# Kernel optimization log

Hardware: AMD Instinct MI355X
Metric: run time of the kernel (lower is better)

Reference implementation:

```python
import jax, jax.numpy as jnp
import numpy as np

B, N, IN_DIM, HID = 16, 1024, 2, 64
GDEP = 2
ALPHA = 3.0                      # DGCRM/DGCN tanh alpha
GC_ALPHA, GC_BETA, GC_GAMMA = 0.05, 0.95, 0.95  # list_weight
HYPER, MID, NODE_DIM = 32, 16, 40
CIN = HID + IN_DIM               # 66
CAT = (GDEP + 1) * CIN           # 198


def setup_inputs() -> dict:
    key = jax.random.key(0)
    ks = jax.random.split(key, 14)
    x = jax.random.normal(ks[0], (B, N, IN_DIM), jnp.float32)
    hidden_state = 0.1 * jax.random.normal(ks[1], (B, N, HID), jnp.float32)
    nodevec1 = jax.random.normal(ks[2], (N, NODE_DIM), jnp.float32)
    nodevec2 = jax.random.normal(ks[3], (N, NODE_DIM), jnp.float32)
    A0 = jax.random.uniform(ks[4], (N, N), jnp.float32)
    A0 = A0 / A0.sum(-1, keepdims=True)
    A1 = jax.random.uniform(ks[5], (N, N), jnp.float32)
    A1 = A1 / A1.sum(-1, keepdims=True)
    s = 0.05  # small init scale
    hyper_W1 = s * jax.random.normal(ks[6], (4, CAT, HYPER), jnp.float32)
    hyper_b1 = jnp.zeros((4, HYPER), jnp.float32)
    hyper_W2 = s * jax.random.normal(ks[7], (4, HYPER, MID), jnp.float32)
    hyper_b2 = jnp.zeros((4, MID), jnp.float32)
    hyper_W3 = s * jax.random.normal(ks[8], (4, MID, NODE_DIM), jnp.float32)
    hyper_b3 = jnp.zeros((4, NODE_DIM), jnp.float32)
    rnn_W = s * jax.random.normal(ks[9], (6, CAT, HID), jnp.float32)
    rnn_b = jnp.zeros((6, HID), jnp.float32)
    return dict(x=x, hidden_state=hidden_state, nodevec1=nodevec1, nodevec2=nodevec2,
                A0=A0, A1=A1, hyper_W1=hyper_W1, hyper_b1=hyper_b1,
                hyper_W2=hyper_W2, hyper_b2=hyper_b2, hyper_W3=hyper_W3,
                hyper_b3=hyper_b3, rnn_W=rnn_W, rnn_b=rnn_b)


def reference(x, hidden_state, nodevec1, nodevec2, A0, A1,
              hyper_W1, hyper_b1, hyper_W2, hyper_b2, hyper_W3, hyper_b3,
              rnn_W, rnn_b):
    def gconv_hyper(inp, adj, i):
        # K-hop diffusion: h = alpha*x + gamma * (h^T adj) over node dim
        h = inp
        outs = [h]
        for _ in range(GDEP):
            h = GC_ALPHA * inp + GC_GAMMA * jnp.einsum('bnc,nm->bmc', h, adj)
            outs.append(h)
        ho = jnp.concatenate(outs, axis=-1)           # [B,N,(gdep+1)*CIN]
        ho = jax.nn.sigmoid(ho @ hyper_W1[i] + hyper_b1[i])
        ho = jax.nn.sigmoid(ho @ hyper_W2[i] + hyper_b2[i])
        return ho @ hyper_W3[i] + hyper_b3[i]         # [B,N,NODE_DIM]

    def gconv_rnn(inp, i):
        # FAITHFUL to source bug: stray leading '+' makes the beta/gamma
        # einsum terms standalone no-op statements, so each hop is h=alpha*x.
        outs = [inp] + [GC_ALPHA * inp] * GDEP
        return jnp.concatenate(outs, axis=-1) @ rnn_W[i] + rnn_b[i]

    # --- DGCN: dynamic adjacency generation ---
    hyper_input = jnp.concatenate((x, hidden_state), axis=-1)  # [B,N,CIN]
    filter1 = gconv_hyper(hyper_input, A0, 0) + gconv_hyper(hyper_input, A1, 1)
    filter2 = gconv_hyper(hyper_input, A0, 2) + gconv_hyper(hyper_input, A1, 3)
    nv1 = jnp.tanh(ALPHA * nodevec1[None] * filter1)  # [B,N,NODE_DIM]
    nv2 = jnp.tanh(ALPHA * nodevec2[None] * filter2)
    a = jnp.einsum('bnd,bmd->bnm', nv1, nv2) - jnp.einsum('bnd,bmd->bnm', nv2, nv1)
    adp_raw = jax.nn.relu(jnp.tanh(ALPHA * a))        # [B,N,N]
    eye = jnp.eye(N, dtype=adp_raw.dtype)
    def norm(adj):
        adj = adj + eye
        return adj / adj.sum(-1, keepdims=True)
    adp = norm(adp_raw)                               # computed as in source
    adpT = norm(jnp.swapaxes(adp_raw, 1, 2))          # (unused downstream due to
    del adp, adpT                                     #  the GConv_RNN source bug)

    # --- GRU-style gating ---
    combined = jnp.concatenate((x, hidden_state), axis=-1)
    z = jax.nn.sigmoid(gconv_rnn(combined, 0) + gconv_rnn(combined, 1))
    r = jax.nn.sigmoid(gconv_rnn(combined, 2) + gconv_rnn(combined, 3))
    candidate = jnp.concatenate((x, r * hidden_state), axis=-1)
    hc = jnp.tanh(gconv_rnn(candidate, 4) + gconv_rnn(candidate, 5))
    h = z * hidden_state + (1.0 - z) * hc             # [B,N,HID]
    return h
```

## Files before the change

### kernel.cpp

```cpp
#include <hip/hip_runtime.h>
#include <math.h>

#define NTOK   16384
#define CIN_   66
#define HID_   64
#define NCH    192
#define TPB    32

__device__ __forceinline__ float fast_sigmoid(float a) {
    return 1.0f / (1.0f + __expf(-a));
}
__device__ __forceinline__ float fast_tanh(float a) {
    return 1.0f - 2.0f / (__expf(2.0f * a) + 1.0f);
}

__global__ void fold_weights(const float* __restrict__ rnn_W,
                             const float* __restrict__ rnn_b,
                             float* __restrict__ Wf,
                             float* __restrict__ bf)
{
    int idx = blockIdx.x * blockDim.x + threadIdx.x;
    if (idx >= CIN_ * NCH) return;
    int k = idx / NCH;
    int c = idx - k * NCH;
    int g = c >> 6;
    int j = c & 63;
    int i0 = 2 * g, i1 = 2 * g + 1;
    const float s = 0.05f;
    float v = 0.0f;
    v += rnn_W[(i0 * 198 + k) * 64 + j]
       + s * (rnn_W[(i0 * 198 + 66 + k) * 64 + j] + rnn_W[(i0 * 198 + 132 + k) * 64 + j]);
    v += rnn_W[(i1 * 198 + k) * 64 + j]
       + s * (rnn_W[(i1 * 198 + 66 + k) * 64 + j] + rnn_W[(i1 * 198 + 132 + k) * 64 + j]);
    Wf[k * NCH + c] = v;
    if (k == 0) bf[c] = rnn_b[i0 * 64 + j] + rnn_b[i1 * 64 + j];
}

__global__ __launch_bounds__(256)
void dgcrm_gru(const float* __restrict__ x,
               const float* __restrict__ h,
               const float* __restrict__ Wf,
               const float* __restrict__ bf,
               float* __restrict__ out)
{
    __shared__ float C[CIN_][TPB + 1];
    __shared__ float D[CIN_][TPB + 1];
    __shared__ float Z[HID_][TPB + 1];

    const int tid = threadIdx.x;
    const int t0  = blockIdx.x * TPB;

    {
        const float4* h4 = (const float4*)(h + (size_t)t0 * HID_);
        #pragma unroll
        for (int r = 0; r < 2; ++r) {
            int i = tid + r * 256;
            float4 v = h4[i];
            int f = i * 4;
            int t = f >> 6;
            int c = f & 63;
            C[2 + c + 0][t] = v.x;
            C[2 + c + 1][t] = v.y;
            C[2 + c + 2][t] = v.z;
            C[2 + c + 3][t] = v.w;
        }
    }
    if (tid < 2 * TPB) {
        int t = tid >> 1, k = tid & 1;
        float v = x[(size_t)(t0 + t) * 2 + k];
        C[k][t] = v;
        D[k][t] = v;
    }
    __syncthreads();

    const int grp  = tid >> 4;
    const int tokA = tid & 15;
    const int tokB = tokA + 16;

    {
        const int ch0 = grp * 8;
        float accA[8], accB[8];
        {
            float4 b0 = *(const float4*)(bf + ch0);
            float4 b1 = *(const float4*)(bf + ch0 + 4);
            accA[0] = b0.x; accA[1] = b0.y; accA[2] = b0.z; accA[3] = b0.w;
            accA[4] = b1.x; accA[5] = b1.y; accA[6] = b1.z; accA[7] = b1.w;
            #pragma unroll
            for (int j = 0; j < 8; ++j) accB[j] = accA[j];
        }
        for (int k = 0; k < CIN_; ++k) {
            float ckA = C[k][tokA];
            float ckB = C[k][tokB];
            const float4* w4 = (const float4*)(Wf + k * NCH + ch0);
            float4 w0 = w4[0];
            float4 w1 = w4[1];
            accA[0] = fmaf(ckA, w0.x, accA[0]);  accB[0] = fmaf(ckB, w0.x, accB[0]);
            accA[1] = fmaf(ckA, w0.y, accA[1]);  accB[1] = fmaf(ckB, w0.y, accB[1]);
            accA[2] = fmaf(ckA, w0.z, accA[2]);  accB[2] = fmaf(ckB, w0.z, accB[2]);
            accA[3] = fmaf(ckA, w0.w, accA[3]);  accB[3] = fmaf(ckB, w0.w, accB[3]);
            accA[4] = fmaf(ckA, w1.x, accA[4]);  accB[4] = fmaf(ckB, w1.x, accB[4]);
            accA[5] = fmaf(ckA, w1.y, accA[5]);  accB[5] = fmaf(ckB, w1.y, accB[5]);
            accA[6] = fmaf(ckA, w1.z, accA[6]);  accB[6] = fmaf(ckB, w1.z, accB[6]);
            accA[7] = fmaf(ckA, w1.w, accA[7]);  accB[7] = fmaf(ckB, w1.w, accB[7]);
        }
        if (grp < 8) {
            #pragma unroll
            for (int j = 0; j < 8; ++j) {
                Z[ch0 + j][tokA] = fast_sigmoid(accA[j]);
                Z[ch0 + j][tokB] = fast_sigmoid(accB[j]);
            }
        } else {
            const int rb = ch0 - 64;
            #pragma unroll
            for (int j = 0; j < 8; ++j) {
                D[2 + rb + j][tokA] = fast_sigmoid(accA[j]) * C[2 + rb + j][tokA];
                D[2 + rb + j][tokB] = fast_sigmoid(accB[j]) * C[2 + rb + j][tokB];
            }
        }
    }
    __syncthreads();

    {
        const int c0 = 128 + grp * 4;
        float accA[4], accB[4];
        {
            float4 b0 = *(const float4*)(bf + c0);
            accA[0] = b0.x; accA[1] = b0.y; accA[2] = b0.z; accA[3] = b0.w;
            #pragma unroll
            for (int j = 0; j < 4; ++j) accB[j] = accA[j];
        }
        for (int k = 0; k < CIN_; ++k) {
            float dkA = D[k][tokA];
            float dkB = D[k][tokB];
            float4 w = *(const float4*)(Wf + k * NCH + c0);
            accA[0] = fmaf(dkA, w.x, accA[0]);  accB[0] = fmaf(dkB, w.x, accB[0]);
            accA[1] = fmaf(dkA, w.y, accA[1]);  accB[1] = fmaf(dkB, w.y, accB[1]);
            accA[2] = fmaf(dkA, w.z, accA[2]);  accB[2] = fmaf(dkB, w.z, accB[2]);
            accA[3] = fmaf(dkA, w.w, accA[3]);  accB[3] = fmaf(dkB, w.w, accB[3]);
        }
        const int hb = grp * 4;
        #pragma unroll
        for (int j = 0; j < 4; ++j) {
            float hcA = fast_tanh(accA[j]);
            float hcB = fast_tanh(accB[j]);
            float zvA = Z[hb + j][tokA];
            float zvB = Z[hb + j][tokB];
            float hvA = C[2 + hb + j][tokA];
            float hvB = C[2 + hb + j][tokB];
            Z[hb + j][tokA] = zvA * hvA + (1.0f - zvA) * hcA;
            Z[hb + j][tokB] = zvB * hvB + (1.0f - zvB) * hcB;
        }
    }
    __syncthreads();

    {
        float4* o4 = (float4*)(out + (size_t)t0 * HID_);
        #pragma unroll
        for (int r = 0; r < 2; ++r) {
            int i = tid + r * 256;
            int f = i * 4;
            int t = f >> 6;
            int c = f & 63;
            float4 v;
            v.x = Z[c + 0][t];
            v.y = Z[c + 1][t];
            v.z = Z[c + 2][t];
            v.w = Z[c + 3][t];
            o4[i] = v;
        }
    }
}

extern "C" void kernel_launch(void* const* d_in, const int* in_sizes, int n_in,
                              void* d_out, int out_size, void* d_ws, size_t ws_size,
                              hipStream_t stream)
{
    const float* x     = (const float*)d_in[0];
    const float* hprev = (const float*)d_in[1];
    const float* rnn_W = (const float*)d_in[12];
    const float* rnn_b = (const float*)d_in[13];

    float* Wf = (float*)d_ws;
    float* bf = Wf + CIN_ * NCH;

    fold_weights<<<(CIN_ * NCH + 255) / 256, 256, 0, stream>>>(rnn_W, rnn_b, Wf, bf);
    dgcrm_gru<<<NTOK / TPB, 256, 0, stream>>>(x, hprev, Wf, bf, (float*)d_out);
}
```

Measured before the change: 102.3 us.

## Switch shared tiles to token-major with float4 access and regroup folded weights per thread group

Shared-memory staging tiles change from channel-major to token-major with a padded row of 68, so hidden-state loads, gate reads and output stores use float4 accesses instead of scalar transposed ones. Input channels are reordered so the 64 hidden channels come first and the two x channels last. The folded weight matrix is split into per-group contiguous blocks to make each thread group's weight reads sequential. This targets LDS instruction count and scattered weight loads, at the cost of more complex indexing and possible LDS bank conflicts from float4 reads across rows.

```diff
diff --git a/kernel.cpp b/kernel.cpp
--- a/kernel.cpp
+++ b/kernel.cpp
@@ -6,6 +6,10 @@
 #define HID_   64
 #define NCH    192
 #define TPB    32
+#define KPAD   68
+
+#define WT1_ELEMS (16 * 66 * 8)
+#define WT2_ELEMS (16 * 66 * 4)
 
 __device__ __forceinline__ float fast_sigmoid(float a) {
     return 1.0f / (1.0f + __expf(-a));
@@ -16,36 +20,50 @@
 
 __global__ void fold_weights(const float* __restrict__ rnn_W,
                              const float* __restrict__ rnn_b,
-                             float* __restrict__ Wf,
+                             float* __restrict__ Wt1,
+                             float* __restrict__ Wt2,
                              float* __restrict__ bf)
 {
     int idx = blockIdx.x * blockDim.x + threadIdx.x;
     if (idx >= CIN_ * NCH) return;
-    int k = idx / NCH;
-    int c = idx - k * NCH;
+    int knew = idx / NCH;
+    int c    = idx - knew * NCH;
+    int korig = (knew < 64) ? (knew + 2) : (knew - 64);
     int g = c >> 6;
     int j = c & 63;
     int i0 = 2 * g, i1 = 2 * g + 1;
     const float s = 0.05f;
     float v = 0.0f;
-    v += rnn_W[(i0 * 198 + k) * 64 + j]
-       + s * (rnn_W[(i0 * 198 + 66 + k) * 64 + j] + rnn_W[(i0 * 198 + 132 + k) * 64 + j]);
-    v += rnn_W[(i1 * 198 + k) * 64 + j]
-       + s * (rnn_W[(i1 * 198 + 66 + k) * 64 + j] + rnn_W[(i1 * 198 + 132 + k) * 64 + j]);
-    Wf[k * NCH + c] = v;
-    if (k == 0) bf[c] = rnn_b[i0 * 64 + j] + rnn_b[i1 * 64 + j];
+    v += rnn_W[(i0 * 198 + korig) * 64 + j]
+       + s * (rnn_W[(i0 * 198 + 66 + korig) * 64 + j] + rnn_W[(i0 * 198 + 132 + korig) * 64 + j]);
+    v += rnn_W[(i1 * 198 + korig) * 64 + j]
+       + s * (rnn_W[(i1 * 198 + 66 + korig) * 64 + j] + rnn_W[(i1 * 198 + 132 + korig) * 64 + j]);
+
+    if (g < 2) {
+        int ch  = c;
+        int grp = ch >> 3;
+        int jj  = ch & 7;
+        Wt1[(grp * CIN_ + knew) * 8 + jj] = v;
+    } else {
+        int ch  = c - 128;
+        int grp = ch >> 2;
+        int jj  = ch & 3;
+        Wt2[(grp * CIN_ + knew) * 4 + jj] = v;
+    }
+    if (knew == 0) bf[c] = rnn_b[i0 * 64 + j] + rnn_b[i1 * 64 + j];
 }
 
 __global__ __launch_bounds__(256)
 void dgcrm_gru(const float* __restrict__ x,
                const float* __restrict__ h,
-               const float* __restrict__ Wf,
+               const float* __restrict__ Wt1,
+               const float* __restrict__ Wt2,
                const float* __restrict__ bf,
                float* __restrict__ out)
 {
-    __shared__ float C[CIN_][TPB + 1];
-    __shared__ float D[CIN_][TPB + 1];
-    __shared__ float Z[HID_][TPB + 1];
+    __shared__ float Cs[TPB][KPAD];
+    __shared__ float Ds[TPB][KPAD];
+    __shared__ float Zs[TPB][KPAD];
 
     const int tid = threadIdx.x;
     const int t0  = blockIdx.x * TPB;
@@ -56,20 +74,16 @@
         for (int r = 0; r < 2; ++r) {
             int i = tid + r * 256;
             float4 v = h4[i];
-            int f = i * 4;
-            int t = f >> 6;
-            int c = f & 63;
-            C[2 + c + 0][t] = v.x;
-            C[2 + c + 1][t] = v.y;
-            C[2 + c + 2][t] = v.z;
-            C[2 + c + 3][t] = v.w;
+            int t = i >> 4;
+            int c = (i * 4) & 63;
+            *(float4*)&Cs[t][c] = v;
         }
     }
     if (tid < 2 * TPB) {
         int t = tid >> 1, k = tid & 1;
         float v = x[(size_t)(t0 + t) * 2 + k];
-        C[k][t] = v;
-        D[k][t] = v;
+        Cs[t][64 + k] = v;
+        Ds[t][64 + k] = v;
     }
     __syncthreads();
 
@@ -79,6 +93,7 @@
 
     {
         const int ch0 = grp * 8;
+        const float* wp = Wt1 + grp * (CIN_ * 8);
         float accA[8], accB[8];
         {
             float4 b0 = *(const float4*)(bf + ch0);
@@ -88,40 +103,81 @@
             #pragma unroll
             for (int j = 0; j < 8; ++j) accB[j] = accA[j];
         }
-        for (int k = 0; k < CIN_; ++k) {
-            float ckA = C[k][tokA];
-            float ckB = C[k][tokB];
-            const float4* w4 = (const float4*)(Wf + k * NCH + ch0);
-            float4 w0 = w4[0];
-            float4 w1 = w4[1];
-            accA[0] = fmaf(ckA, w0.x, accA[0]);  accB[0] = fmaf(ckB, w0.x, accB[0]);
-            accA[1] = fmaf(ckA, w0.y, accA[1]);  accB[1] = fmaf(ckB, w0.y, accB[1]);
-            accA[2] = fmaf(ckA, w0.z, accA[2]);  accB[2] = fmaf(ckB, w0.z, accB[2]);
-            accA[3] = fmaf(ckA, w0.w, accA[3]);  accB[3] = fmaf(ckB, w0.w, accB[3]);
-            accA[4] = fmaf(ckA, w1.x, accA[4]);  accB[4] = fmaf(ckB, w1.x, accB[4]);
-            accA[5] = fmaf(ckA, w1.y, accA[5]);  accB[5] = fmaf(ckB, w1.y, accB[5]);
-            accA[6] = fmaf(ckA, w1.z, accA[6]);  accB[6] = fmaf(ckB, w1.z, accB[6]);
-            accA[7] = fmaf(ckA, w1.w, accA[7]);  accB[7] = fmaf(ckB, w1.w, accB[7]);
+        #pragma unroll
+        for (int kb = 0; kb < 16; ++kb) {
+            float4 a4 = *(const float4*)&Cs[tokA][4 * kb];
+            float4 b4 = *(const float4*)&Cs[tokB][4 * kb];
+            float ca[4] = {a4.x, a4.y, a4.z, a4.w};
+            float cb[4] = {b4.x, b4.y, b4.z, b4.w};
+            #pragma unroll
+            for (int j = 0; j < 4; ++j) {
+                float4 w0 = *(const float4*)(wp + (4 * kb + j) * 8);
+                float4 w1 = *(const float4*)(wp + (4 * kb + j) * 8 + 4);
+                accA[0] = fmaf(ca[j], w0.x, accA[0]);  accB[0] = fmaf(cb[j], w0.x, accB[0]);
+                accA[1] = fmaf(ca[j], w0.y, accA[1]);  accB[1] = fmaf(cb[j], w0.y, accB[1]);
+                accA[2] = fmaf(ca[j], w0.z, accA[2]);  accB[2] = fmaf(cb[j], w0.z, accB[2]);
+                accA[3] = fmaf(ca[j], w0.w, accA[3]);  accB[3] = fmaf(cb[j], w0.w, accB[3]);
+                accA[4] = fmaf(ca[j], w1.x, accA[4]);  accB[4] = fmaf(cb[j], w1.x, accB[4]);
+                accA[5] = fmaf(ca[j], w1.y, accA[5]);  accB[5] = fmaf(cb[j], w1.y, accB[5]);
+                accA[6] = fmaf(ca[j], w1.z, accA[6]);  accB[6] = fmaf(cb[j], w1.z, accB[6]);
+                accA[7] = fmaf(ca[j], w1.w, accA[7]);  accB[7] = fmaf(cb[j], w1.w, accB[7]);
+            }
+        }
+        {
+            float a64 = Cs[tokA][64], a65 = Cs[tokA][65];
+            float b64 = Cs[tokB][64], b65 = Cs[tokB][65];
+            float4 u0 = *(const float4*)(wp + 64 * 8);
+            float4 u1 = *(const float4*)(wp + 64 * 8 + 4);
+            float4 v0 = *(const float4*)(wp + 65 * 8);
+            float4 v1 = *(const float4*)(wp + 65 * 8 + 4);
+            float wu[8] = {u0.x,u0.y,u0.z,u0.w,u1.x,u1.y,u1.z,u1.w};
+            float wv[8] = {v0.x,v0.y,v0.z,v0.w,v1.x,v1.y,v1.z,v1.w};
+            #pragma unroll
+            for (int j = 0; j < 8; ++j) {
+                accA[j] = fmaf(a64, wu[j], fmaf(a65, wv[j], accA[j]));
+                accB[j] = fmaf(b64, wu[j], fmaf(b65, wv[j], accB[j]));
+            }
         }
         if (grp < 8) {
-            #pragma unroll
-            for (int j = 0; j < 8; ++j) {
-                Z[ch0 + j][tokA] = fast_sigmoid(accA[j]);
-                Z[ch0 + j][tokB] = fast_sigmoid(accB[j]);
-            }
+            float4 za0, za1, zb0, zb1;
+            za0.x = fast_sigmoid(accA[0]); za0.y = fast_sigmoid(accA[1]);
+            za0.z = fast_sigmoid(accA[2]); za0.w = fast_sigmoid(accA[3]);
+            za1.x = fast_sigmoid(accA[4]); za1.y = fast_sigmoid(accA[5]);
+            za1.z = fast_sigmoid(accA[6]); za1.w = fast_sigmoid(accA[7]);
+            zb0.x = fast_sigmoid(accB[0]); zb0.y = fast_sigmoid(accB[1]);
+            zb0.z = fast_sigmoid(accB[2]); zb0.w = fast_sigmoid(accB[3]);
+            zb1.x = fast_sigmoid(accB[4]); zb1.y = fast_sigmoid(accB[5]);
+            zb1.z = fast_sigmoid(accB[6]); zb1.w = fast_sigmoid(accB[7]);
+            *(float4*)&Zs[tokA][ch0]     = za0;
+            *(float4*)&Zs[tokA][ch0 + 4] = za1;
+            *(float4*)&Zs[tokB][ch0]     = zb0;
+            *(float4*)&Zs[tokB][ch0 + 4] = zb1;
         } else {
             const int rb = ch0 - 64;
-            #pragma unroll
-            for (int j = 0; j < 8; ++j) {
-                D[2 + rb + j][tokA] = fast_sigmoid(accA[j]) * C[2 + rb + j][tokA];
-                D[2 + rb + j][tokB] = fast_sigmoid(accB[j]) * C[2 + rb + j][tokB];
-            }
+            float4 ha0 = *(const float4*)&Cs[tokA][rb];
+            float4 ha1 = *(const float4*)&Cs[tokA][rb + 4];
+            float4 hb0 = *(const float4*)&Cs[tokB][rb];
+            float4 hb1 = *(const float4*)&Cs[tokB][rb + 4];
+            float4 da0, da1, db0, db1;
+            da0.x = fast_sigmoid(accA[0]) * ha0.x;  da0.y = fast_sigmoid(accA[1]) * ha0.y;
+            da0.z = fast_sigmoid(accA[2]) * ha0.z;  da0.w = fast_sigmoid(accA[3]) * ha0.w;
+            da1.x = fast_sigmoid(accA[4]) * ha1.x;  da1.y = fast_sigmoid(accA[5]) * ha1.y;
+            da1.z = fast_sigmoid(accA[6]) * ha1.z;  da1.w = fast_sigmoid(accA[7]) * ha1.w;
+            db0.x = fast_sigmoid(accB[0]) * hb0.x;  db0.y = fast_sigmoid(accB[1]) * hb0.y;
+            db0.z = fast_sigmoid(accB[2]) * hb0.z;  db0.w = fast_sigmoid(accB[3]) * hb0.w;
+            db1.x = fast_sigmoid(accB[4]) * hb1.x;  db1.y = fast_sigmoid(accB[5]) * hb1.y;
+            db1.z = fast_sigmoid(accB[6]) * hb1.z;  db1.w = fast_sigmoid(accB[7]) * hb1.w;
+            *(float4*)&Ds[tokA][rb]     = da0;
+            *(float4*)&Ds[tokA][rb + 4] = da1;
+            *(float4*)&Ds[tokB][rb]     = db0;
+            *(float4*)&Ds[tokB][rb + 4] = db1;
         }
     }
     __syncthreads();
 
     {
         const int c0 = 128 + grp * 4;
+        const float* wp = Wt2 + grp * (CIN_ * 4);
         float accA[4], accB[4];
         {
             float4 b0 = *(const float4*)(bf + c0);
@@ -129,27 +185,50 @@
             #pragma unroll
             for (int j = 0; j < 4; ++j) accB[j] = accA[j];
         }
-        for (int k = 0; k < CIN_; ++k) {
-            float dkA = D[k][tokA];
-            float dkB = D[k][tokB];
-            float4 w = *(const float4*)(Wf + k * NCH + c0);
-            accA[0] = fmaf(dkA, w.x, accA[0]);  accB[0] = fmaf(dkB, w.x, accB[0]);
-            accA[1] = fmaf(dkA, w.y, accA[1]);  accB[1] = fmaf(dkB, w.y, accB[1]);
-            accA[2] = fmaf(dkA, w.z, accA[2]);  accB[2] = fmaf(dkB, w.z, accB[2]);
-            accA[3] = fmaf(dkA, w.w, accA[3]);  accB[3] = fmaf(dkB, w.w, accB[3]);
+        #pragma unroll
+        for (int kb = 0; kb < 16; ++kb) {
+            float4 a4 = *(const float4*)&Ds[tokA][4 * kb];
+            float4 b4 = *(const float4*)&Ds[tokB][4 * kb];
+            float ca[4] = {a4.x, a4.y, a4.z, a4.w};
+            float cb[4] = {b4.x, b4.y, b4.z, b4.w};
+            #pragma unroll
+            for (int j = 0; j < 4; ++j) {
+                float4 w = *(const float4*)(wp + (4 * kb + j) * 4);
+                accA[0] = fmaf(ca[j], w.x, accA[0]);  accB[0] = fmaf(cb[j], w.x, accB[0]);
+                accA[1] = fmaf(ca[j], w.y, accA[1]);  accB[1] = fmaf(cb[j], w.y, accB[1]);
+                accA[2] = fmaf(ca[j], w.z, accA[2]);  accB[2] = fmaf(cb[j], w.z, accB[2]);
+                accA[3] = fmaf(ca[j], w.w, accA[3]);  accB[3] = fmaf(cb[j], w.w, accB[3]);
+            }
+        }
+        {
+            float a64 = Ds[tokA][64], a65 = Ds[tokA][65];
+            float b64 = Ds[tokB][64], b65 = Ds[tokB][65];
+            float4 u = *(const float4*)(wp + 64 * 4);
+            float4 v = *(const float4*)(wp + 65 * 4);
+            float wu[4] = {u.x, u.y, u.z, u.w};
+            float wv[4] = {v.x, v.y, v.z, v.w};
+            #pragma unroll
+            for (int j = 0; j < 4; ++j) {
+                accA[j] = fmaf(a64, wu[j], fmaf(a65, wv[j], accA[j]));
+                accB[j] = fmaf(b64, wu[j], fmaf(b65, wv[j], accB[j]));
+            }
         }
         const int hb = grp * 4;
-        #pragma unroll
-        for (int j = 0; j < 4; ++j) {
-            float hcA = fast_tanh(accA[j]);
-            float hcB = fast_tanh(accB[j]);
-            float zvA = Z[hb + j][tokA];
-            float zvB = Z[hb + j][tokB];
-            float hvA = C[2 + hb + j][tokA];
-            float hvB = C[2 + hb + j][tokB];
-            Z[hb + j][tokA] = zvA * hvA + (1.0f - zvA) * hcA;
-            Z[hb + j][tokB] = zvB * hvB + (1.0f - zvB) * hcB;
-        }
+        float4 zA = *(const float4*)&Zs[tokA][hb];
+        float4 zB = *(const float4*)&Zs[tokB][hb];
+        float4 hA = *(const float4*)&Cs[tokA][hb];
+        float4 hB = *(const float4*)&Cs[tokB][hb];
+        float4 oA, oB;
+        oA.x = zA.x * hA.x + (1.0f - zA.x) * fast_tanh(accA[0]);
+        oA.y = zA.y * hA.y + (1.0f - zA.y) * fast_tanh(accA[1]);
+        oA.z = zA.z * hA.z + (1.0f - zA.z) * fast_tanh(accA[2]);
+        oA.w = zA.w * hA.w + (1.0f - zA.w) * fast_tanh(accA[3]);
+        oB.x = zB.x * hB.x + (1.0f - zB.x) * fast_tanh(accB[0]);
+        oB.y = zB.y * hB.y + (1.0f - zB.y) * fast_tanh(accB[1]);
+        oB.z = zB.z * hB.z + (1.0f - zB.z) * fast_tanh(accB[2]);
+        oB.w = zB.w * hB.w + (1.0f - zB.w) * fast_tanh(accB[3]);
+        *(float4*)&Zs[tokA][hb] = oA;
+        *(float4*)&Zs[tokB][hb] = oB;
     }
     __syncthreads();
 
@@ -158,15 +237,9 @@
         #pragma unroll
         for (int r = 0; r < 2; ++r) {
             int i = tid + r * 256;
-            int f = i * 4;
-            int t = f >> 6;
-            int c = f & 63;
-            float4 v;
-            v.x = Z[c + 0][t];
-            v.y = Z[c + 1][t];
-            v.z = Z[c + 2][t];
-            v.w = Z[c + 3][t];
-            o4[i] = v;
+            int t = i >> 4;
+            int c = (i * 4) & 63;
+            o4[i] = *(const float4*)&Zs[t][c];
         }
     }
 }
@@ -180,9 +253,10 @@
     const float* rnn_W = (const float*)d_in[12];
     const float* rnn_b = (const float*)d_in[13];
 
-    float* Wf = (float*)d_ws;
-    float* bf = Wf + CIN_ * NCH;
-
-    fold_weights<<<(CIN_ * NCH + 255) / 256, 256, 0, stream>>>(rnn_W, rnn_b, Wf, bf);
-    dgcrm_gru<<<NTOK / TPB, 256, 0, stream>>>(x, hprev, Wf, bf, (float*)d_out);
-}
+    float* Wt1 = (float*)d_ws;
+    float* Wt2 = Wt1 + WT1_ELEMS;
+    float* bf  = Wt2 + WT2_ELEMS;
+
+    fold_weights<<<(CIN_ * NCH + 255) / 256, 256, 0, stream>>>(rnn_W, rnn_b, Wt1, Wt2, bf);
+    dgcrm_gru<<<NTOK / TPB, 256, 0, stream>>>(x, hprev, Wt1, Wt2, bf, (float*)d_out);
+}
```

Result: faster. 99.23 us (-3.0%).
